# Optimization experiments

Measured on AMD Instinct MI355X. Metric: run time of the kernel, lower is better.

The kernel has to match this reference:

```python
import jax, jax.numpy as jnp
import numpy as np

CLASSES = (32, 32)
SUPERCLASSES = 8
OVERALL = CLASSES[0] * CLASSES[1]
CLASS_FACTOR = OVERALL // SUPERCLASSES


def lrelu(x):
    return jax.nn.leaky_relu(x, 0.01)


def conv1x1(x, w, b):
    # x: [B,C,H,W], w: [O,C], b: [O]
    return jnp.einsum('oc,bchw->bohw', w, x) + b[None, :, None, None]


def cond_mul(x, inds, W, b):
    # x: [N,I], inds: [N] int, W: [K,I,O], b: [K,O]
    return jnp.einsum('ni,nio->no', x, W[inds]) + b[inds]


def setup_inputs() -> dict:
    key = jax.random.key(0)
    ks = jax.random.split(key, 24)
    s = 0.05
    d = {}
    d['x_in'] = jax.random.normal(ks[0], (1, 128, 192, 256), dtype=jnp.float32)
    # mask branch
    d['Wm1'] = jax.random.normal(ks[1], (32, 128)) * s
    d['bm1'] = jnp.zeros((32,), jnp.float32)
    d['Wm2'] = jax.random.normal(ks[2], (16, 32)) * s
    d['bm2'] = jnp.zeros((16,), jnp.float32)
    d['Wm3'] = jax.random.normal(ks[3], (1, 16)) * s
    d['bm3'] = jnp.zeros((1,), jnp.float32)
    # classification branch
    d['Wcl1'] = jax.random.normal(ks[4], (128, 128)) * s
    d['bcl1'] = jnp.zeros((128,), jnp.float32)
    d['Wcl21'] = jax.random.normal(ks[5], (128, 128)) * s
    d['bcl21'] = jnp.zeros((128,), jnp.float32)
    d['Wcl31'] = jax.random.normal(ks[6], (32, 128)) * s
    d['bcl31'] = jnp.zeros((32,), jnp.float32)
    d['Wcl22'] = jax.random.normal(ks[7], (CLASSES[0], 128, 32)) * s  # CondMul
    d['bcl22'] = jnp.zeros((CLASSES[0], 32), jnp.float32)
    d['Wcl32'] = jax.random.normal(ks[8], (CLASSES[0], 32, CLASSES[1])) * s
    d['bcl32'] = jnp.zeros((CLASSES[0], CLASSES[1]), jnp.float32)
    d['Wr1'] = jax.random.normal(ks[9], (128, 128)) * s
    d['br1'] = jnp.zeros((128,), jnp.float32)
    d['Wr2'] = jax.random.normal(ks[10], (SUPERCLASSES, 128, 32)) * s
    d['br2'] = jnp.zeros((SUPERCLASSES, 32), jnp.float32)
    d['Wr3'] = jax.random.normal(ks[11], (OVERALL, 32, 1)) * s
    d['br3'] = jnp.zeros((OVERALL, 1), jnp.float32)
    return d


def reference(x_in, Wm1, bm1, Wm2, bm2, Wm3, bm3,
              Wcl1, bcl1, Wcl21, bcl21, Wcl31, bcl31,
              Wcl22, bcl22, Wcl32, bcl32,
              Wr1, br1, Wr2, br2, Wr3, br3):
    B = x_in.shape[0]
    # mask branch
    m = lrelu(conv1x1(x_in, Wm1, bm1))
    m = lrelu(conv1x1(m, Wm2, bm2))
    mask = lrelu(conv1x1(m, Wm3, bm3))
    # classification branch
    x = lrelu(conv1x1(x_in, Wcl1, bcl1))          # [B,128,H,W]
    # torch: transpose(1,3) -> [B,W,H,C], flatten
    x_l = jnp.transpose(x, (0, 3, 2, 1)).reshape(-1, x.shape[1])
    x2 = lrelu(conv1x1(x, Wcl21, bcl21))
    cl1 = conv1x1(x2, Wcl31, bcl31)               # [B,classes0,H,W]
    inds1 = jnp.argmax(cl1, axis=1).reshape(-1).astype(jnp.int32)  # [N] (B,H,W order)
    h = lrelu(cond_mul(x_l, inds1, Wcl22, bcl22))  # [N,32]
    h = cond_mul(h, inds1, Wcl32, bcl32)           # [N,classes1]
    inds2 = jnp.argmax(h, axis=1).astype(jnp.int32)
    inds = inds1 * CLASSES[1] + inds2
    inds_r = jnp.clip(inds, 0, OVERALL - 1).astype(jnp.int32)
    inds_super = jnp.clip(inds_r // CLASS_FACTOR, 0, SUPERCLASSES - 1)
    r = lrelu(conv1x1(x_in, Wr1, br1))
    r_l = jnp.transpose(r, (0, 3, 2, 1)).reshape(-1, r.shape[1])
    r2 = lrelu(cond_mul(r_l, inds_super, Wr2, br2))  # [N,32]
    regression = cond_mul(r2, inds_r, Wr3, br3)      # [N,1]
    regression = regression.reshape(B, 1, 1, -1)
    inds = inds.reshape(regression.shape)
    x_real = (inds.astype(jnp.float32) + regression) * (1.0 / float(OVERALL))
    return (x_real, mask)
```

## Files before the change

### kernel.cpp

```cpp
#include <hip/hip_runtime.h>

#define HH 192
#define WW 256
#define NPIX (HH*WW)
#define NSEG (NPIX/64)

__device__ __forceinline__ float lrelu(float v) { return v > 0.0f ? v : 0.01f * v; }

__global__ __launch_bounds__(256, 3) void k_fused1(
    const float* __restrict__ X,
    const float* __restrict__ Wcl1, const float* __restrict__ bcl1,
    const float* __restrict__ Wr1,  const float* __restrict__ br1,
    const float* __restrict__ Wm1,  const float* __restrict__ bm1,
    const float* __restrict__ Wm2,  const float* __restrict__ bm2,
    const float* __restrict__ Wm3,  const float* __restrict__ bm3,
    float* __restrict__ x_t, float* __restrict__ r_t,
    float* __restrict__ out)
{
    __shared__ float As[16][132];
    __shared__ float Ws[16][132];
    __shared__ float m1buf[128][33];
    const int tid = threadIdx.x;
    const int q0  = blockIdx.x * 128;

    if (blockIdx.y == 2) {
        const int tc = tid & 31;
        const int tr = tid >> 5;
        float acc[4][4];
        #pragma unroll
        for (int i = 0; i < 4; ++i)
            #pragma unroll
            for (int j = 0; j < 4; ++j)
                acc[i][j] = bm1[tr * 4 + j];

        for (int k0 = 0; k0 < 128; k0 += 16) {
            #pragma unroll
            for (int p = 0; p < 2; ++p) {
                int lin = p * 1024 + tid * 4;
                int kk = lin >> 7, px = lin & 127;
                float4 v = *(const float4*)(X + (k0 + kk) * NPIX + q0 + px);
                *(float4*)(&As[kk][px]) = v;
            }
            if (tid < 128) {
                int row = tid >> 2, kc = (tid & 3) * 4;
                float4 v = *(const float4*)(Wm1 + row * 128 + k0 + kc);
                Ws[kc + 0][row] = v.x; Ws[kc + 1][row] = v.y;
                Ws[kc + 2][row] = v.z; Ws[kc + 3][row] = v.w;
            }
            __syncthreads();
            #pragma unroll
            for (int kk = 0; kk < 16; ++kk) {
                float4 a = *(const float4*)(&As[kk][tc * 4]);
                float4 w = *(const float4*)(&Ws[kk][tr * 4]);
                float av[4] = {a.x,a.y,a.z,a.w};
                float wv[4] = {w.x,w.y,w.z,w.w};
                #pragma unroll
                for (int i = 0; i < 4; ++i)
                    #pragma unroll
                    for (int j = 0; j < 4; ++j)
                        acc[i][j] = fmaf(av[i], wv[j], acc[i][j]);
            }
            __syncthreads();
        }
        #pragma unroll
        for (int i = 0; i < 4; ++i)
            #pragma unroll
            for (int j = 0; j < 4; ++j)
                m1buf[tc * 4 + i][tr * 4 + j] = lrelu(acc[i][j]);
        __syncthreads();
        if (tid < 128) {
            float m3 = bm3[0];
            #pragma unroll 2
            for (int j = 0; j < 16; ++j) {
                float s = bm2[j];
                #pragma unroll
                for (int k = 0; k < 32; ++k)
                    s = fmaf(Wm2[j * 32 + k], m1buf[tid][k], s);
                m3 = fmaf(Wm3[j], lrelu(s), m3);
            }
            out[NPIX + q0 + tid] = lrelu(m3);
        }
        return;
    }

    const float* __restrict__ W    = (blockIdx.y == 0) ? Wcl1 : Wr1;
    const float* __restrict__ bias = (blockIdx.y == 0) ? bcl1 : br1;
    float* __restrict__ outp       = (blockIdx.y == 0) ? x_t : r_t;

    const int tc = tid & 15;
    const int tr = tid >> 4;

    float acc[8][8];
    #pragma unroll
    for (int i = 0; i < 8; ++i)
        #pragma unroll
        for (int j = 0; j < 8; ++j)
            acc[i][j] = bias[(j >> 2) * 64 + tr * 4 + (j & 3)];

    for (int k0 = 0; k0 < 128; k0 += 16) {
        #pragma unroll
        for (int p = 0; p < 2; ++p) {
            int lin = p * 1024 + tid * 4;
            int kk = lin >> 7, px = lin & 127;
            float4 v = *(const float4*)(X + (k0 + kk) * NPIX + q0 + px);
            *(float4*)(&As[kk][px]) = v;
        }
        #pragma unroll
        for (int p = 0; p < 2; ++p) {
            int lin = p * 1024 + tid * 4;
            int row = lin >> 4, kc = lin & 15;
            float4 v = *(const float4*)(W + row * 128 + k0 + kc);
            Ws[kc + 0][row] = v.x; Ws[kc + 1][row] = v.y;
            Ws[kc + 2][row] = v.z; Ws[kc + 3][row] = v.w;
        }
        __syncthreads();
        #pragma unroll
        for (int kk = 0; kk < 16; ++kk) {
            float4 a0 = *(const float4*)(&As[kk][tc * 4]);
            float4 a1 = *(const float4*)(&As[kk][64 + tc * 4]);
            float4 w0 = *(const float4*)(&Ws[kk][tr * 4]);
            float4 w1 = *(const float4*)(&Ws[kk][64 + tr * 4]);
            float av[8] = {a0.x,a0.y,a0.z,a0.w,a1.x,a1.y,a1.z,a1.w};
            float wv[8] = {w0.x,w0.y,w0.z,w0.w,w1.x,w1.y,w1.z,w1.w};
            #pragma unroll
            for (int i = 0; i < 8; ++i)
                #pragma unroll
                for (int j = 0; j < 8; ++j)
                    acc[i][j] = fmaf(av[i], wv[j], acc[i][j]);
        }
        __syncthreads();
    }

    #pragma unroll
    for (int i = 0; i < 8; ++i) {
        int px = (i >> 2) * 64 + tc * 4 + (i & 3);
        int q  = q0 + px;
        int np = (q & 255) * 192 + (q >> 8);
        float* op = outp + (size_t)np * 128;
        #pragma unroll
        for (int jg = 0; jg < 2; ++jg) {
            float4 o;
            o.x = lrelu(acc[i][jg*4+0]); o.y = lrelu(acc[i][jg*4+1]);
            o.z = lrelu(acc[i][jg*4+2]); o.w = lrelu(acc[i][jg*4+3]);
            *(float4*)(op + jg * 64 + tr * 4) = o;
        }
    }
}

__global__ __launch_bounds__(256, 2) void k1b(
    const float* __restrict__ x_t,
    const float* __restrict__ Wcl21, const float* __restrict__ bcl21,
    const float* __restrict__ Wcl31, const float* __restrict__ bcl31,
    int* __restrict__ inds1_q)
{
    __shared__ float smem[12672];
    float (*As)[132]     = (float(*)[132])smem;
    float (*Ws)[132]     = (float(*)[132])(smem + 2112);
    float (*W31)[132]    = (float(*)[132])smem;
    float (*x2t)[132]    = (float(*)[132])(smem + 4224);
    float (*cl1buf)[33]  = (float(*)[33]) (smem + 4224);

    const int tid = threadIdx.x;
    const int n0  = blockIdx.x * 128;
    const int tcA = tid & 15, trA = tid >> 4;
    const int tcB = tid & 31, trB = tid >> 5;

    float acc[8][8];
    #pragma unroll
    for (int i = 0; i < 8; ++i)
        #pragma unroll
        for (int j = 0; j < 8; ++j)
            acc[i][j] = bcl21[(j >> 2) * 64 + trA * 4 + (j & 3)];

    for (int k0 = 0; k0 < 128; k0 += 16) {
        #pragma unroll
        for (int p = 0; p < 2; ++p) {
            int lin = p * 1024 + tid * 4;
            int px = lin >> 4, kc = lin & 15;
            float4 v = *(const float4*)(x_t + (size_t)(n0 + px) * 128 + k0 + kc);
            As[kc + 0][px] = v.x; As[kc + 1][px] = v.y;
            As[kc + 2][px] = v.z; As[kc + 3][px] = v.w;
        }
        #pragma unroll
        for (int p = 0; p < 2; ++p) {
            int lin = p * 256 + tid;
            int r = lin >> 2, kc = (lin & 3) * 4;
            float4 v = *(const float4*)(Wcl21 + r * 128 + k0 + kc);
            Ws[kc + 0][r] = v.x; Ws[kc + 1][r] = v.y;
            Ws[kc + 2][r] = v.z; Ws[kc + 3][r] = v.w;
        }
        __syncthreads();
        #pragma unroll
        for (int kk = 0; kk < 16; ++kk) {
            float4 a0 = *(const float4*)(&As[kk][tcA * 4]);
            float4 a1 = *(const float4*)(&As[kk][64 + tcA * 4]);
            float4 w0 = *(const float4*)(&Ws[kk][trA * 4]);
            float4 w1 = *(const float4*)(&Ws[kk][64 + trA * 4]);
            float av[8] = {a0.x,a0.y,a0.z,a0.w,a1.x,a1.y,a1.z,a1.w};
            float wv[8] = {w0.x,w0.y,w0.z,w0.w,w1.x,w1.y,w1.z,w1.w};
            #pragma unroll
            for (int i = 0; i < 8; ++i)
                #pragma unroll
                for (int j = 0; j < 8; ++j)
                    acc[i][j] = fmaf(av[i], wv[j], acc[i][j]);
        }
        __syncthreads();
    }

    float accB[4][4];
    #pragma unroll
    for (int i = 0; i < 4; ++i)
        #pragma unroll
        for (int j = 0; j < 4; ++j)
            accB[i][j] = bcl31[trB * 4 + j];

    #pragma unroll
    for (int p = 0; p < 4; ++p) {
        int lin = p * 1024 + tid * 4;
        int row = lin >> 7, kc = lin & 127;
        *(float4*)(&W31[row][kc]) = *(const float4*)(Wcl31 + row * 128 + kc);
    }
    #pragma unroll
    for (int j = 0; j < 4; ++j) {
        int row = trA * 4 + j;
        #pragma unroll
        for (int gi = 0; gi < 2; ++gi) {
            float4 o;
            o.x = lrelu(acc[gi*4+0][j]); o.y = lrelu(acc[gi*4+1][j]);
            o.z = lrelu(acc[gi*4+2][j]); o.w = lrelu(acc[gi*4+3][j]);
            *(float4*)(&x2t[row][gi * 64 + tcA * 4]) = o;
        }
    }
    __syncthreads();
    for (int k = 0; k < 64; ++k) {
        float4 a = *(const float4*)(&x2t[k][tcB * 4]);
        float av[4] = {a.x,a.y,a.z,a.w};
        float wv[4];
        #pragma unroll
        for (int j = 0; j < 4; ++j) wv[j] = W31[trB * 4 + j][k];
        #pragma unroll
        for (int i = 0; i < 4; ++i)
            #pragma unroll
            for (int j = 0; j < 4; ++j)
                accB[i][j] = fmaf(av[i], wv[j], accB[i][j]);
    }
    __syncthreads();
    #pragma unroll
    for (int j = 0; j < 4; ++j) {
        int row = trA * 4 + j;
        #pragma unroll
        for (int gi = 0; gi < 2; ++gi) {
            float4 o;
            o.x = lrelu(acc[gi*4+0][4+j]); o.y = lrelu(acc[gi*4+1][4+j]);
            o.z = lrelu(acc[gi*4+2][4+j]); o.w = lrelu(acc[gi*4+3][4+j]);
            *(float4*)(&x2t[row][gi * 64 + tcA * 4]) = o;
        }
    }
    __syncthreads();
    for (int k = 0; k < 64; ++k) {
        float4 a = *(const float4*)(&x2t[k][tcB * 4]);
        float av[4] = {a.x,a.y,a.z,a.w};
        float wv[4];
        #pragma unroll
        for (int j = 0; j < 4; ++j) wv[j] = W31[trB * 4 + j][64 + k];
        #pragma unroll
        for (int i = 0; i < 4; ++i)
            #pragma unroll
            for (int j = 0; j < 4; ++j)
                accB[i][j] = fmaf(av[i], wv[j], accB[i][j]);
    }
    __syncthreads();

    #pragma unroll
    for (int i = 0; i < 4; ++i)
        #pragma unroll
        for (int j = 0; j < 4; ++j)
            cl1buf[tcB * 4 + i][trB * 4 + j] = accB[i][j];
    __syncthreads();
    if (tid < 128) {
        float bv = cl1buf[tid][0]; int bi = 0;
        #pragma unroll
        for (int c = 1; c < 32; ++c) {
            float v = cl1buf[tid][c];
            if (v > bv) { bv = v; bi = c; }
        }
        int n = n0 + tid;
        int w = n / 192, hh = n - w * 192;
        inds1_q[hh * 256 + w] = bi;
    }
}

__global__ void k_hist(const int* __restrict__ inds1_q, int* __restrict__ bh) {
    int tid = threadIdx.x;
    int n = blockIdx.x * 256 + tid;
    int key = inds1_q[n];
    int lane = tid & 63;
    int cnt = 0;
    for (int k = 0; k < 32; ++k) {
        unsigned long long m = __ballot(key == k);
        if (lane == k) cnt = __popcll(m);
    }
    if (lane < 32) bh[(n >> 6) * 32 + lane] = cnt;
}

__global__ void k_scanA(const int* __restrict__ bh, int* __restrict__ ebb,
                        int* __restrict__ total) {
    __shared__ int s[256];
    const int k = blockIdx.x, t = threadIdx.x;
    int v0 = bh[(t * 3 + 0) * 32 + k];
    int v1 = bh[(t * 3 + 1) * 32 + k];
    int v2 = bh[(t * 3 + 2) * 32 + k];
    int sum = v0 + v1 + v2;
    s[t] = sum; __syncthreads();
    for (int d = 1; d < 256; d <<= 1) {
        int x = (t >= d) ? s[t - d] : 0;
        __syncthreads();
        s[t] += x;
        __syncthreads();
    }
    int ex = s[t] - sum;
    ebb[(t * 3 + 0) * 32 + k] = ex;
    ebb[(t * 3 + 1) * 32 + k] = ex + v0;
    ebb[(t * 3 + 2) * 32 + k] = ex + v0 + v1;
    if (t == 255) total[k] = s[255];
}

__global__ void k_scatter2(const int* __restrict__ inds1_q,
                           const int* __restrict__ ebb,
                           const int* __restrict__ total,
                           int* __restrict__ order)
{
    __shared__ int ttot[32];
    const int tid = threadIdx.x;
    if (tid < 32) ttot[tid] = total[tid];
    __syncthreads();
    int n = blockIdx.x * 256 + tid;
    int key = inds1_q[n];
    int lane = tid & 63;
    unsigned long long peers = 0;
    for (int k = 0; k < 32; ++k) {
        unsigned long long m = __ballot(key == k);
        if (key == k) peers = m;
    }
    int rank = __popcll(peers & ((1ull << lane) - 1ull));
    int cbase = 0;
    #pragma unroll
    for (int k = 0; k < 32; ++k) cbase += (k < key) ? ttot[k] : 0;
    order[cbase + ebb[(n >> 6) * 32 + key] + rank] = n;
}

__global__ __launch_bounds__(256, 4) void k2h(
    const float* __restrict__ x_t,
    const float* __restrict__ Wcl22, const float* __restrict__ bcl22,
    const float* __restrict__ Wcl32, const float* __restrict__ bcl32,
    const int* __restrict__ total, const int* __restrict__ order,
    int* __restrict__ ind_ord)
{
    __shared__ float Was[4096];
    __shared__ float Wbs[1024];
    __shared__ int cpre[33];
    __shared__ int cbase[33];
    __shared__ int ttot[32];

    const int tid = threadIdx.x;
    if (tid < 32) ttot[tid] = total[tid];
    __syncthreads();
    if (tid == 0) {
        int s = 0, cb = 0;
        for (int k = 0; k < 32; ++k) {
            cpre[k] = s; cbase[k] = cb;
            int c = ttot[k];
            s += (c + 255) >> 8;
            cb += c;
        }
        cpre[32] = s; cbase[32] = cb;
    }
    __syncthreads();
    const int ci = blockIdx.x;
    if (ci >= cpre[32]) return;
    int cls = 0;
    while (cpre[cls + 1] <= ci) ++cls;
    const int st   = (ci - cpre[cls]) * 256;
    const int npx  = min(256, ttot[cls] - st);
    const int base = cbase[cls] + st;

    {
        const float4* ws = (const float4*)(Wcl22 + cls * 4096);
        #pragma unroll
        for (int j = 0; j < 4; ++j) ((float4*)Was)[j * 256 + tid] = ws[j * 256 + tid];
        ((float4*)Wbs)[tid] = ((const float4*)(Wcl32 + cls * 1024))[tid];
    }
    __syncthreads();

    const int m = order[base + min(tid, npx - 1)];
    const float4* xp = (const float4*)(x_t + (size_t)m * 128);

    float h[32];
    #pragma unroll
    for (int j = 0; j < 32; ++j) h[j] = bcl22[cls * 32 + j];
    #pragma unroll 2
    for (int c4 = 0; c4 < 32; ++c4) {
        float4 xv = xp[c4];
        float xa[4] = {xv.x, xv.y, xv.z, xv.w};
        #pragma unroll
        for (int cc = 0; cc < 4; ++cc) {
            const float* wr = &Was[(c4 * 4 + cc) * 32];
            #pragma unroll
            for (int j = 0; j < 32; ++j) h[j] = fmaf(xa[cc], wr[j], h[j]);
        }
    }
    #pragma unroll
    for (int j = 0; j < 32; ++j) h[j] = lrelu(h[j]);

    float g[32];
    #pragma unroll
    for (int j = 0; j < 32; ++j) g[j] = bcl32[cls * 32 + j];
    #pragma unroll 2
    for (int c = 0; c < 32; ++c) {
        float hv = h[c];
        const float* wr = &Wbs[c * 32];
        #pragma unroll
        for (int j = 0; j < 32; ++j) g[j] = fmaf(hv, wr[j], g[j]);
    }
    float bv = g[0]; int bi = 0;
    #pragma unroll
    for (int j = 1; j < 32; ++j)
        if (g[j] > bv) { bv = g[j]; bi = j; }
    if (tid < npx) ind_ord[base + tid] = cls * 32 + bi;
}

__global__ __launch_bounds__(256, 4) void k2r(
    const float* __restrict__ r_t,
    const float* __restrict__ Wr2,  const float* __restrict__ br2,
    const float* __restrict__ Wr3,  const float* __restrict__ br3,
    const int* __restrict__ total, const int* __restrict__ order,
    const int* __restrict__ ind_ord,
    float* __restrict__ out)
{
    __shared__ float Wcs[4096];
    __shared__ int cpre[33];
    __shared__ int cbase[33];
    __shared__ int ttot[32];

    const int tid = threadIdx.x;
    if (tid < 32) ttot[tid] = total[tid];
    __syncthreads();
    if (tid == 0) {
        int s = 0, cb = 0;
        for (int k = 0; k < 32; ++k) {
            cpre[k] = s; cbase[k] = cb;
            int c = ttot[k];
            s += (c + 255) >> 8;
            cb += c;
        }
        cpre[32] = s; cbase[32] = cb;
    }
    __syncthreads();
    const int ci = blockIdx.x;
    if (ci >= cpre[32]) return;
    int cls = 0;
    while (cpre[cls + 1] <= ci) ++cls;
    const int st   = (ci - cpre[cls]) * 256;
    const int npx  = min(256, ttot[cls] - st);
    const int base = cbase[cls] + st;
    const int sup  = cls >> 2;

    {
        const float4* ws = (const float4*)(Wr2 + sup * 4096);
        #pragma unroll
        for (int j = 0; j < 4; ++j) ((float4*)Wcs)[j * 256 + tid] = ws[j * 256 + tid];
    }
    __syncthreads();

    const int li  = min(tid, npx - 1);
    const int m   = order[base + li];
    const int ind = ind_ord[base + li];
    const float4* rp = (const float4*)(r_t + (size_t)m * 128);

    float r2[32];
    #pragma unroll
    for (int j = 0; j < 32; ++j) r2[j] = br2[sup * 32 + j];
    #pragma unroll 2
    for (int c4 = 0; c4 < 32; ++c4) {
        float4 rv = rp[c4];
        float ra[4] = {rv.x, rv.y, rv.z, rv.w};
        #pragma unroll
        for (int cc = 0; cc < 4; ++cc) {
            const float* wr = &Wcs[(c4 * 4 + cc) * 32];
            #pragma unroll
            for (int j = 0; j < 32; ++j) r2[j] = fmaf(ra[cc], wr[j], r2[j]);
        }
    }

    float reg = br3[ind];
    const float* __restrict__ w3 = Wr3 + ind * 32;
    #pragma unroll
    for (int j = 0; j < 32; ++j) reg = fmaf(lrelu(r2[j]), w3[j], reg);

    if (tid < npx) out[m] = ((float)ind + reg) * (1.0f / 1024.0f);
}

extern "C" void kernel_launch(void* const* d_in, const int* in_sizes, int n_in,
                              void* d_out, int out_size, void* d_ws, size_t ws_size,
                              hipStream_t stream)
{
    const float* X     = (const float*)d_in[0];
    const float* Wm1   = (const float*)d_in[1];
    const float* bm1   = (const float*)d_in[2];
    const float* Wm2   = (const float*)d_in[3];
    const float* bm2   = (const float*)d_in[4];
    const float* Wm3   = (const float*)d_in[5];
    const float* bm3   = (const float*)d_in[6];
    const float* Wcl1  = (const float*)d_in[7];
    const float* bcl1  = (const float*)d_in[8];
    const float* Wcl21 = (const float*)d_in[9];
    const float* bcl21 = (const float*)d_in[10];
    const float* Wcl31 = (const float*)d_in[11];
    const float* bcl31 = (const float*)d_in[12];
    const float* Wcl22 = (const float*)d_in[13];
    const float* bcl22 = (const float*)d_in[14];
    const float* Wcl32 = (const float*)d_in[15];
    const float* bcl32 = (const float*)d_in[16];
    const float* Wr1   = (const float*)d_in[17];
    const float* br1   = (const float*)d_in[18];
    const float* Wr2   = (const float*)d_in[19];
    const float* br2   = (const float*)d_in[20];
    const float* Wr3   = (const float*)d_in[21];
    const float* br3   = (const float*)d_in[22];
    float* out = (float*)d_out;

    float* x_t   = (float*)d_ws;
    float* r_t   = x_t + (size_t)NPIX * 128;
    int* inds1_q = (int*)(r_t + (size_t)NPIX * 128);
    int* order   = inds1_q + NPIX;
    int* ind_ord = order + NPIX;
    int* bh      = ind_ord + NPIX;
    int* ebb     = bh + NSEG * 32;
    int* total   = ebb + NSEG * 32;

    k_fused1<<<dim3(NPIX / 128, 3), 256, 0, stream>>>(X, Wcl1, bcl1, Wr1, br1,
                                                      Wm1, bm1, Wm2, bm2, Wm3, bm3,
                                                      x_t, r_t, out);
    k1b<<<NPIX / 128, 256, 0, stream>>>(x_t, Wcl21, bcl21, Wcl31, bcl31, inds1_q);
    k_hist<<<NPIX / 256, 256, 0, stream>>>(inds1_q, bh);
    k_scanA<<<32, 256, 0, stream>>>(bh, ebb, total);
    k_scatter2<<<NPIX / 256, 256, 0, stream>>>(inds1_q, ebb, total, order);
    k2h<<<224, 256, 0, stream>>>(x_t, Wcl22, bcl22, Wcl32, bcl32, total, order, ind_ord);
    k2r<<<224, 256, 0, stream>>>(r_t, Wr2, br2, Wr3, br3, total, order, ind_ord, out);
}
```

Measured before the change: 241.9 us.

## Split per-pixel CondMul channel reduction across four lanes in k2h and k2r

```diff
diff --git a/kernel.cpp b/kernel.cpp
--- a/kernel.cpp
+++ b/kernel.cpp
@@ -356,7 +356,7 @@
     const int* __restrict__ total, const int* __restrict__ order,
     int* __restrict__ ind_ord)
 {
-    __shared__ float Was[4096];
+    __shared__ float Was[128 * 33];
     __shared__ float Wbs[1024];
     __shared__ int cpre[33];
     __shared__ int cbase[33];
@@ -370,7 +370,7 @@
         for (int k = 0; k < 32; ++k) {
             cpre[k] = s; cbase[k] = cb;
             int c = ttot[k];
-            s += (c + 255) >> 8;
+            s += (c + 63) >> 6;
             cb += c;
         }
         cpre[32] = s; cbase[32] = cb;
@@ -380,53 +380,75 @@
     if (ci >= cpre[32]) return;
     int cls = 0;
     while (cpre[cls + 1] <= ci) ++cls;
-    const int st   = (ci - cpre[cls]) * 256;
-    const int npx  = min(256, ttot[cls] - st);
+    const int st   = (ci - cpre[cls]) * 64;
+    const int npx  = min(64, ttot[cls] - st);
     const int base = cbase[cls] + st;
 
     {
-        const float4* ws = (const float4*)(Wcl22 + cls * 4096);
-        #pragma unroll
-        for (int j = 0; j < 4; ++j) ((float4*)Was)[j * 256 + tid] = ws[j * 256 + tid];
+        const float* ws = Wcl22 + cls * 4096;
+        #pragma unroll
+        for (int p = 0; p < 4; ++p) {
+            int q = p * 1024 + tid * 4;
+            int r = q >> 5, j = q & 31;
+            float4 v = *(const float4*)(ws + q);
+            Was[r * 33 + j + 0] = v.x; Was[r * 33 + j + 1] = v.y;
+            Was[r * 33 + j + 2] = v.z; Was[r * 33 + j + 3] = v.w;
+        }
         ((float4*)Wbs)[tid] = ((const float4*)(Wcl32 + cls * 1024))[tid];
     }
     __syncthreads();
 
-    const int m = order[base + min(tid, npx - 1)];
+    const int pw   = (tid >> 6) * 16 + (tid & 15);
+    const int part = (tid >> 4) & 3;
+    const int li = min(pw, npx - 1);
+    const int m  = order[base + li];
     const float4* xp = (const float4*)(x_t + (size_t)m * 128);
 
     float h[32];
     #pragma unroll
-    for (int j = 0; j < 32; ++j) h[j] = bcl22[cls * 32 + j];
+    for (int j = 0; j < 32; ++j) h[j] = 0.0f;
     #pragma unroll 2
-    for (int c4 = 0; c4 < 32; ++c4) {
+    for (int c4i = 0; c4i < 8; ++c4i) {
+        int c4 = c4i * 4 + part;
         float4 xv = xp[c4];
         float xa[4] = {xv.x, xv.y, xv.z, xv.w};
         #pragma unroll
         for (int cc = 0; cc < 4; ++cc) {
-            const float* wr = &Was[(c4 * 4 + cc) * 32];
+            const float* wr = &Was[(c4 * 4 + cc) * 33];
             #pragma unroll
             for (int j = 0; j < 32; ++j) h[j] = fmaf(xa[cc], wr[j], h[j]);
         }
     }
     #pragma unroll
-    for (int j = 0; j < 32; ++j) h[j] = lrelu(h[j]);
-
-    float g[32];
-    #pragma unroll
-    for (int j = 0; j < 32; ++j) g[j] = bcl32[cls * 32 + j];
-    #pragma unroll 2
+    for (int j = 0; j < 32; ++j) {
+        h[j] += __shfl_xor(h[j], 16, 64);
+        h[j] += __shfl_xor(h[j], 32, 64);
+        h[j] = lrelu(h[j] + bcl22[cls * 32 + j]);
+    }
+
+    float g[8];
+    #pragma unroll
+    for (int jj = 0; jj < 8; ++jj) g[jj] = bcl32[cls * 32 + part * 8 + jj];
+    #pragma unroll 4
     for (int c = 0; c < 32; ++c) {
         float hv = h[c];
-        const float* wr = &Wbs[c * 32];
-        #pragma unroll
-        for (int j = 0; j < 32; ++j) g[j] = fmaf(hv, wr[j], g[j]);
-    }
-    float bv = g[0]; int bi = 0;
-    #pragma unroll
-    for (int j = 1; j < 32; ++j)
-        if (g[j] > bv) { bv = g[j]; bi = j; }
-    if (tid < npx) ind_ord[base + tid] = cls * 32 + bi;
+        const float* wr = &Wbs[c * 32 + part * 8];
+        #pragma unroll
+        for (int jj = 0; jj < 8; ++jj) g[jj] = fmaf(hv, wr[jj], g[jj]);
+    }
+    float bv = g[0]; int bi = part * 8;
+    #pragma unroll
+    for (int jj = 1; jj < 8; ++jj)
+        if (g[jj] > bv) { bv = g[jj]; bi = part * 8 + jj; }
+    {
+        float ov = __shfl_xor(bv, 16, 64);
+        int   oi = __shfl_xor(bi, 16, 64);
+        if (ov > bv || (ov == bv && oi < bi)) { bv = ov; bi = oi; }
+        ov = __shfl_xor(bv, 32, 64);
+        oi = __shfl_xor(bi, 32, 64);
+        if (ov > bv || (ov == bv && oi < bi)) { bv = ov; bi = oi; }
+    }
+    if (part == 0 && pw < npx) ind_ord[base + pw] = cls * 32 + bi;
 }
 
 __global__ __launch_bounds__(256, 4) void k2r(
@@ -437,7 +459,7 @@
     const int* __restrict__ ind_ord,
     float* __restrict__ out)
 {
-    __shared__ float Wcs[4096];
+    __shared__ float Wcs[128 * 33];
     __shared__ int cpre[33];
     __shared__ int cbase[33];
     __shared__ int ttot[32];
@@ -450,7 +472,7 @@
         for (int k = 0; k < 32; ++k) {
             cpre[k] = s; cbase[k] = cb;
             int c = ttot[k];
-            s += (c + 255) >> 8;
+            s += (c + 63) >> 6;
             cb += c;
         }
         cpre[32] = s; cbase[32] = cb;
@@ -460,44 +482,63 @@
     if (ci >= cpre[32]) return;
     int cls = 0;
     while (cpre[cls + 1] <= ci) ++cls;
-    const int st   = (ci - cpre[cls]) * 256;
-    const int npx  = min(256, ttot[cls] - st);
+    const int st   = (ci - cpre[cls]) * 64;
+    const int npx  = min(64, ttot[cls] - st);
     const int base = cbase[cls] + st;
     const int sup  = cls >> 2;
 
     {
-        const float4* ws = (const float4*)(Wr2 + sup * 4096);
-        #pragma unroll
-        for (int j = 0; j < 4; ++j) ((float4*)Wcs)[j * 256 + tid] = ws[j * 256 + tid];
-    }
-    __syncthreads();
-
-    const int li  = min(tid, npx - 1);
+        const float* ws = Wr2 + sup * 4096;
+        #pragma unroll
+        for (int p = 0; p < 4; ++p) {
+            int q = p * 1024 + tid * 4;
+            int r = q >> 5, j = q & 31;
+            float4 v = *(const float4*)(ws + q);
+            Wcs[r * 33 + j + 0] = v.x; Wcs[r * 33 + j + 1] = v.y;
+            Wcs[r * 33 + j + 2] = v.z; Wcs[r * 33 + j + 3] = v.w;
+        }
+    }
+    __syncthreads();
+
+    const int pw   = (tid >> 6) * 16 + (tid & 15);
+    const int part = (tid >> 4) & 3;
+    const int li  = min(pw, npx - 1);
     const int m   = order[base + li];
     const int ind = ind_ord[base + li];
     const float4* rp = (const float4*)(r_t + (size_t)m * 128);
 
     float r2[32];
     #pragma unroll
-    for (int j = 0; j < 32; ++j) r2[j] = br2[sup * 32 + j];
+    for (int j = 0; j < 32; ++j) r2[j] = 0.0f;
     #pragma unroll 2
-    for (int c4 = 0; c4 < 32; ++c4) {
+    for (int c4i = 0; c4i < 8; ++c4i) {
+        int c4 = c4i * 4 + part;
         float4 rv = rp[c4];
         float ra[4] = {rv.x, rv.y, rv.z, rv.w};
         #pragma unroll
         for (int cc = 0; cc < 4; ++cc) {
-            const float* wr = &Wcs[(c4 * 4 + cc) * 32];
+            const float* wr = &Wcs[(c4 * 4 + cc) * 33];
             #pragma unroll
             for (int j = 0; j < 32; ++j) r2[j] = fmaf(ra[cc], wr[j], r2[j]);
         }
     }
-
-    float reg = br3[ind];
-    const float* __restrict__ w3 = Wr3 + ind * 32;
-    #pragma unroll
-    for (int j = 0; j < 32; ++j) reg = fmaf(lrelu(r2[j]), w3[j], reg);
-
-    if (tid < npx) out[m] = ((float)ind + reg) * (1.0f / 1024.0f);
+    #pragma unroll
+    for (int j = 0; j < 32; ++j) {
+        r2[j] += __shfl_xor(r2[j], 16, 64);
+        r2[j] += __shfl_xor(r2[j], 32, 64);
+        r2[j] += br2[sup * 32 + j];
+    }
+
+    float s = 0.0f;
+    const float* __restrict__ w3 = Wr3 + ind * 32 + part * 8;
+    #pragma unroll
+    for (int jj = 0; jj < 8; ++jj)
+        s = fmaf(lrelu(r2[part * 8 + jj]), w3[jj], s);
+    s += __shfl_xor(s, 16, 64);
+    s += __shfl_xor(s, 32, 64);
+
+    if (part == 0 && pw < npx)
+        out[m] = ((float)ind + (br3[ind] + s)) * (1.0f / 1024.0f);
 }
 
 extern "C" void kernel_launch(void* const* d_in, const int* in_sizes, int n_in,
@@ -545,6 +586,6 @@
     k_hist<<<NPIX / 256, 256, 0, stream>>>(inds1_q, bh);
     k_scanA<<<32, 256, 0, stream>>>(bh, ebb, total);
     k_scatter2<<<NPIX / 256, 256, 0, stream>>>(inds1_q, ebb, total, order);
-    k2h<<<224, 256, 0, stream>>>(x_t, Wcl22, bcl22, Wcl32, bcl32, total, order, ind_ord);
-    k2r<<<224, 256, 0, stream>>>(r_t, Wr2, br2, Wr3, br3, total, order, ind_ord, out);
-}
+    k2h<<<800, 256, 0, stream>>>(x_t, Wcl22, bcl22, Wcl32, bcl32, total, order, ind_ord);
+    k2r<<<800, 256, 0, stream>>>(r_t, Wr2, br2, Wr3, br3, total, order, ind_ord, out);
+}
```

New measurement: 244.0 us. No clear change (+0.9%).
